# Kernel optimization log

Hardware: AMD Instinct MI355X
Metric: run time of the kernel (lower is better)

## Reference

```python
import jax, jax.numpy as jnp
import numpy as np

NQ = 20
P_MAX = 480 * 640 - 1  # hardcoded clamp in original module


def make_quantizer_params(nq=NQ, mn=0.0, mx=1.0):
    # Replicates APLoss.__init__ conv1d weight/bias initialization.
    a = (nq - 1) / (mx - mn)
    w = np.concatenate([-a * np.ones(nq), a * np.ones(nq)]).astype(np.float32)
    b = np.concatenate([a * mn + np.arange(nq, 0, -1),
                        np.arange(2 - nq, 2, 1) - a * mn]).astype(np.float32)
    w[0] = w[-1] = 0.0
    b[0] = b[-1] = 1.0
    return jnp.asarray(w), jnp.asarray(b)


def setup_inputs() -> dict:
    key = jax.random.key(0)
    k1, k2, k3, k4, k5 = jax.random.split(key, 5)
    P, D, N, NEG = 307200, 64, 20000, 80
    qw, qb = make_quantizer_params()
    return {
        "descriptors1": jax.random.normal(k1, (1, P, D), dtype=jnp.float32),
        "descriptors2": jax.random.normal(k2, (1, P, D), dtype=jnp.float32),
        "qw": qw,
        "qb": qb,
        "matches_1": jax.random.randint(k3, (N,), 0, P),
        "matches_2": jax.random.randint(k4, (N,), 0, P),
        "offsets": jax.random.randint(k5, (NEG,), 0, 640),
    }


def reference(descriptors1, descriptors2, qw, qb, matches_1, matches_2, offsets):
    nq = qw.shape[0] // 2
    d1 = descriptors1[0]  # (P, D)
    d2 = descriptors2[0]  # (P, D)

    # negative indices: offset positive matches, clamp to valid pixel range
    non_m2 = jnp.clip(matches_2[:, None] + offsets[None, :], 0, P_MAX)  # (N, NEG)

    a1 = d1[matches_1]                                  # (N, D)
    pos = jnp.sum(a1 * d2[matches_2], axis=-1)          # (N,)
    neg = jnp.einsum('nd,nmd->nm', a1, d2[non_m2])      # (N, NEG)

    scores = jnp.concatenate([pos[:, None], neg], axis=1)   # (N, M), M = 1+NEG
    label = jnp.zeros_like(scores).at[:, 0].set(1.0)         # (N, M)

    # soft quantizer: 1x1 conv == per-bin affine; min of two halves, relu
    x = scores[:, None, :]                                   # (N, 1, M)
    q = jnp.minimum(qw[:nq, None] * x + qb[:nq, None],
                    qw[nq:, None] * x + qb[nq:, None])
    q = jnp.maximum(q, 0.0)                                  # (N, nq, M)

    nbs = q.sum(axis=-1)                                     # (N, nq)
    rec = (q * label[:, None, :]).sum(axis=-1)               # (N, nq)
    prec = jnp.cumsum(rec, axis=-1) / (1e-16 + jnp.cumsum(nbs, axis=-1))
    rec = rec / rec.sum(axis=-1, keepdims=True)
    ap = (prec * rec).sum(axis=-1)                           # (N,)
    return (1.0 - ap).mean()
```

## Files before the change

kernel.cpp:

```cpp
#include <hip/hip_runtime.h>

#define DIM 64

__global__ __launch_bounds__(256) void pixel_ap_main(
    const float* __restrict__ d1, const float* __restrict__ d2,
    const float* __restrict__ qw, const float* __restrict__ qb,
    const int* __restrict__ m1, const int* __restrict__ m2,
    const int* __restrict__ offs,
    float* __restrict__ partial, int P, int NEG, int NQ2)
{
    const int n   = blockIdx.x;
    const int tid = threadIdx.x;
    const int nq  = NQ2 >> 1;
    const int M   = NEG + 1;

    __shared__ float s_a1[DIM];
    __shared__ int   s_off[128];
    __shared__ float s_scores[1 + 128];
    __shared__ float s_nbs[32];
    __shared__ float s_rec[32];

    const int i1 = m1[n];
    const int i2 = m2[n];

    if (tid < DIM) s_a1[tid] = d1[(size_t)i1 * DIM + tid];
    if (tid >= 64 && tid - 64 < NEG) s_off[tid - 64] = offs[tid - 64];
    __syncthreads();

    const int g = tid >> 4;
    const int l = tid & 15;
    const float4 a4 = ((const float4*)s_a1)[l];

    for (int j = g; j < M; j += 16) {
        int row = (j == 0) ? i2 : min(i2 + s_off[j - 1], P - 1);
        const float4 b4 = ((const float4*)(d2 + (size_t)row * DIM))[l];
        float s = a4.x * b4.x + a4.y * b4.y + a4.z * b4.z + a4.w * b4.w;
        s += __shfl_xor(s, 1);
        s += __shfl_xor(s, 2);
        s += __shfl_xor(s, 4);
        s += __shfl_xor(s, 8);
        if (l == 0) s_scores[j] = s;
    }
    __syncthreads();

    if (tid < nq) {
        const float wlo = qw[tid],      whi = qw[nq + tid];
        const float blo = qb[tid],      bhi = qb[nq + tid];
        float nbs = 0.f, rec = 0.f;
        for (int j = 0; j < M; ++j) {
            const float x = s_scores[j];
            float q = fminf(wlo * x + blo, whi * x + bhi);
            q = fmaxf(q, 0.f);
            nbs += q;
            if (j == 0) rec = q;
        }
        s_nbs[tid] = nbs;
        s_rec[tid] = rec;
    }
    __syncthreads();

    if (tid == 0) {
        float cr = 0.f, cn = 0.f, ap = 0.f, rsum = 0.f;
        for (int k = 0; k < nq; ++k) {
            const float r = s_rec[k];
            cr += r;
            cn += s_nbs[k];
            const float prec = cr / (1e-16f + cn);
            ap   += prec * r;
            rsum += r;
        }
        ap = ap / rsum;
        partial[n] = 1.0f - ap;
    }
}

__global__ __launch_bounds__(256) void pixel_ap_reduce(
    const float* __restrict__ partial, float* __restrict__ out, int N)
{
    float s = 0.f;
    for (int i = threadIdx.x; i < N; i += 256) s += partial[i];
    for (int off = 32; off >= 1; off >>= 1) s += __shfl_down(s, off);
    __shared__ float s_w[4];
    const int wid = threadIdx.x >> 6;
    if ((threadIdx.x & 63) == 0) s_w[wid] = s;
    __syncthreads();
    if (threadIdx.x == 0) {
        float t = s_w[0] + s_w[1] + s_w[2] + s_w[3];
        out[0] = t / (float)N;
    }
}

extern "C" void kernel_launch(void* const* d_in, const int* in_sizes, int n_in,
                              void* d_out, int out_size, void* d_ws, size_t ws_size,
                              hipStream_t stream) {
    const float* d1   = (const float*)d_in[0];
    const float* d2   = (const float*)d_in[1];
    const float* qw   = (const float*)d_in[2];
    const float* qb   = (const float*)d_in[3];
    const int*   m1   = (const int*)d_in[4];
    const int*   m2   = (const int*)d_in[5];
    const int*   offs = (const int*)d_in[6];

    const int N    = in_sizes[4];
    const int P    = in_sizes[0] / DIM;
    const int NEG  = in_sizes[6];
    const int NQ2  = in_sizes[2];

    float* partial = (float*)d_ws;

    pixel_ap_main<<<N, 256, 0, stream>>>(d1, d2, qw, qb, m1, m2, offs,
                                         partial, P, NEG, NQ2);
    pixel_ap_reduce<<<1, 256, 0, stream>>>(partial, (float*)d_out, N);
}
```

Before: 235.6 us.

## Sort matches by pixel bucket, closed-form AP quantizer, batched loads, two-stage reduce

```diff
diff --git a/kernel.cpp b/kernel.cpp
--- a/kernel.cpp
+++ b/kernel.cpp
@@ -1,93 +1,164 @@
 #include <hip/hip_runtime.h>
 
 #define DIM 64
+
+
+__global__ __launch_bounds__(256) void k_zero(int* __restrict__ cnt, int nbuck) {
+    int i = blockIdx.x * 256 + threadIdx.x;
+    if (i < nbuck) cnt[i] = 0;
+}
+
+__global__ __launch_bounds__(256) void k_hist(const int* __restrict__ m2,
+                                              int* __restrict__ cnt, int N) {
+    int n = blockIdx.x * 256 + threadIdx.x;
+    if (n < N) atomicAdd(&cnt[m2[n] >> 7], 1);
+}
+
+__global__ __launch_bounds__(256) void k_scan(int* __restrict__ cnt, int nbuck) {
+    __shared__ int s[256];
+    const int tid = threadIdx.x;
+    const int base = tid * 10;
+    int loc[10];
+    int sum = 0;
+    #pragma unroll
+    for (int i = 0; i < 10; ++i) {
+        int idx = base + i;
+        int v = (idx < nbuck) ? cnt[idx] : 0;
+        loc[i] = sum;
+        sum += v;
+    }
+    s[tid] = sum;
+    __syncthreads();
+    for (int off = 1; off < 256; off <<= 1) {
+        int v = (tid >= off) ? s[tid - off] : 0;
+        __syncthreads();
+        s[tid] += v;
+        __syncthreads();
+    }
+    const int excl = (tid > 0) ? s[tid - 1] : 0;
+    #pragma unroll
+    for (int i = 0; i < 10; ++i) {
+        int idx = base + i;
+        if (idx < nbuck) cnt[idx] = excl + loc[i];
+    }
+}
+
+__global__ __launch_bounds__(256) void k_scatter(const int* __restrict__ m2,
+                                                 int* __restrict__ cnt,
+                                                 int* __restrict__ perm, int N) {
+    int n = blockIdx.x * 256 + threadIdx.x;
+    if (n < N) {
+        int pos = atomicAdd(&cnt[m2[n] >> 7], 1);
+        perm[pos] = n;
+    }
+}
+
 
 __global__ __launch_bounds__(256) void pixel_ap_main(
     const float* __restrict__ d1, const float* __restrict__ d2,
     const float* __restrict__ qw, const float* __restrict__ qb,
     const int* __restrict__ m1, const int* __restrict__ m2,
-    const int* __restrict__ offs,
+    const int* __restrict__ offs, const int* __restrict__ perm,
     float* __restrict__ partial, int P, int NEG, int NQ2)
 {
-    const int n   = blockIdx.x;
     const int tid = threadIdx.x;
     const int nq  = NQ2 >> 1;
     const int M   = NEG + 1;
 
     __shared__ float s_a1[DIM];
     __shared__ int   s_off[128];
-    __shared__ float s_scores[1 + 128];
-    __shared__ float s_nbs[32];
-    __shared__ float s_rec[32];
+    __shared__ float s_scores[160];
+    __shared__ float s_red[8];
 
+    const int n  = perm[blockIdx.x];
     const int i1 = m1[n];
     const int i2 = m2[n];
 
     if (tid < DIM) s_a1[tid] = d1[(size_t)i1 * DIM + tid];
-    if (tid >= 64 && tid - 64 < NEG) s_off[tid - 64] = offs[tid - 64];
+    if (tid >= 64 && tid < 64 + NEG) s_off[tid - 64] = offs[tid - 64];
     __syncthreads();
 
     const int g = tid >> 4;
     const int l = tid & 15;
     const float4 a4 = ((const float4*)s_a1)[l];
 
-    for (int j = g; j < M; j += 16) {
-        int row = (j == 0) ? i2 : min(i2 + s_off[j - 1], P - 1);
-        const float4 b4 = ((const float4*)(d2 + (size_t)row * DIM))[l];
-        float s = a4.x * b4.x + a4.y * b4.y + a4.z * b4.z + a4.w * b4.w;
-        s += __shfl_xor(s, 1);
-        s += __shfl_xor(s, 2);
-        s += __shfl_xor(s, 4);
-        s += __shfl_xor(s, 8);
-        if (l == 0) s_scores[j] = s;
+    float4 bv[6];
+    #pragma unroll
+    for (int t = 0; t < 6; ++t) {
+        const int j = g + 16 * t;
+        if (j < M) {
+            const int row = (j == 0) ? i2 : min(i2 + s_off[j - 1], P - 1);
+            bv[t] = ((const float4*)(d2 + (size_t)row * DIM))[l];
+        }
+    }
+    #pragma unroll
+    for (int t = 0; t < 6; ++t) {
+        const int j = g + 16 * t;
+        if (j < M) {
+            float s = bv[t].x * a4.x + bv[t].y * a4.y + bv[t].z * a4.z + bv[t].w * a4.w;
+            s += __shfl_xor(s, 1);
+            s += __shfl_xor(s, 2);
+            s += __shfl_xor(s, 4);
+            s += __shfl_xor(s, 8);
+            if (l == 0) s_scores[j] = s;
+        }
     }
     __syncthreads();
 
-    if (tid < nq) {
-        const float wlo = qw[tid],      whi = qw[nq + tid];
-        const float blo = qb[tid],      bhi = qb[nq + tid];
-        float nbs = 0.f, rec = 0.f;
-        for (int j = 0; j < M; ++j) {
-            const float x = s_scores[j];
-            float q = fminf(wlo * x + blo, whi * x + bhi);
-            q = fmaxf(q, 0.f);
-            nbs += q;
-            if (j == 0) rec = q;
-        }
-        s_nbs[tid] = nbs;
-        s_rec[tid] = rec;
+    const float a_scale = qw[nq];
+    const float amn     = qb[nq - 1] - 1.0f;
+    const float ulim    = (float)(nq - 1);
+
+    const float xp = s_scores[0];
+    const float up = fminf(fmaxf(a_scale * xp - amn, 0.0f), ulim);
+    const float ip = floorf(up);
+    const float fp = up - ip;
+
+    float n1 = 0.0f, n2 = 0.0f;
+    if (tid < M) {
+        const float x = s_scores[tid];
+        const float u = fminf(fmaxf(a_scale * x - amn, 0.0f), ulim);
+        const float fi = floorf(u);
+        const float f  = u - fi;
+        n2 = (fi >= ip)        ? 1.0f : ((fi == ip - 1.0f) ? f : 0.0f);
+        n1 = (fi >= ip + 1.0f) ? 1.0f : ((fi == ip)        ? f : 0.0f);
     }
+    #pragma unroll
+    for (int off = 32; off >= 1; off >>= 1) {
+        n1 += __shfl_down(n1, off);
+        n2 += __shfl_down(n2, off);
+    }
+    const int wid = tid >> 6;
+    if ((tid & 63) == 0) { s_red[wid] = n1; s_red[4 + wid] = n2; }
     __syncthreads();
-
     if (tid == 0) {
-        float cr = 0.f, cn = 0.f, ap = 0.f, rsum = 0.f;
-        for (int k = 0; k < nq; ++k) {
-            const float r = s_rec[k];
-            cr += r;
-            cn += s_nbs[k];
-            const float prec = cr / (1e-16f + cn);
-            ap   += prec * r;
-            rsum += r;
-        }
-        ap = ap / rsum;
+        const float N1 = s_red[0] + s_red[1] + s_red[2] + s_red[3];
+        const float N2 = s_red[4] + s_red[5] + s_red[6] + s_red[7];
+        const float ap = fp * fp / (1e-16f + N1) + (1.0f - fp) / (1e-16f + N2);
         partial[n] = 1.0f - ap;
     }
 }
 
-__global__ __launch_bounds__(256) void pixel_ap_reduce(
-    const float* __restrict__ partial, float* __restrict__ out, int N)
-{
-    float s = 0.f;
-    for (int i = threadIdx.x; i < N; i += 256) s += partial[i];
+
+__global__ __launch_bounds__(256) void k_reduce1(const float* __restrict__ partial,
+                                                 float* __restrict__ partial2, int N) {
+    float s = 0.0f;
+    for (int i = blockIdx.x * 256 + threadIdx.x; i < N; i += gridDim.x * 256) s += partial[i];
+    #pragma unroll
     for (int off = 32; off >= 1; off >>= 1) s += __shfl_down(s, off);
     __shared__ float s_w[4];
-    const int wid = threadIdx.x >> 6;
-    if ((threadIdx.x & 63) == 0) s_w[wid] = s;
+    if ((threadIdx.x & 63) == 0) s_w[threadIdx.x >> 6] = s;
     __syncthreads();
-    if (threadIdx.x == 0) {
-        float t = s_w[0] + s_w[1] + s_w[2] + s_w[3];
-        out[0] = t / (float)N;
-    }
+    if (threadIdx.x == 0) partial2[blockIdx.x] = s_w[0] + s_w[1] + s_w[2] + s_w[3];
+}
+
+__global__ __launch_bounds__(64) void k_reduce2(const float* __restrict__ partial2,
+                                                float* __restrict__ out, int nb, int N) {
+    float s = 0.0f;
+    for (int i = threadIdx.x; i < nb; i += 64) s += partial2[i];
+    #pragma unroll
+    for (int off = 32; off >= 1; off >>= 1) s += __shfl_down(s, off);
+    if (threadIdx.x == 0) out[0] = s / (float)N;
 }
 
 extern "C" void kernel_launch(void* const* d_in, const int* in_sizes, int n_in,
@@ -105,10 +176,24 @@
     const int P    = in_sizes[0] / DIM;
     const int NEG  = in_sizes[6];
     const int NQ2  = in_sizes[2];
+    const int nbuck = (P + 127) >> 7;
 
-    float* partial = (float*)d_ws;
+    int*   cnt      = (int*)d_ws;
+    int*   perm     = cnt + nbuck;
+    float* partial  = (float*)(perm + N);
+    float* partial2 = partial + N;
+    const int RB = 80;
 
-    pixel_ap_main<<<N, 256, 0, stream>>>(d1, d2, qw, qb, m1, m2, offs,
+    const int nblk = (N + 255) / 256;
+
+    k_zero   <<<(nbuck + 255) / 256, 256, 0, stream>>>(cnt, nbuck);
+    k_hist   <<<nblk, 256, 0, stream>>>(m2, cnt, N);
+    k_scan   <<<1, 256, 0, stream>>>(cnt, nbuck);
+    k_scatter<<<nblk, 256, 0, stream>>>(m2, cnt, perm, N);
+
+    pixel_ap_main<<<N, 256, 0, stream>>>(d1, d2, qw, qb, m1, m2, offs, perm,
                                          partial, P, NEG, NQ2);
-    pixel_ap_reduce<<<1, 256, 0, stream>>>(partial, (float*)d_out, N);
+
+    k_reduce1<<<RB, 256, 0, stream>>>(partial, partial2, N);
+    k_reduce2<<<1, 64, 0, stream>>>(partial2, (float*)d_out, RB, N);
 }
```

After: 203.7 us. 1.16x faster.
